# Optimization experiments

Hardware: AMD Instinct MI355X
Metric: run time of the kernel (lower is better)

Reference implementation:

```python
import jax, jax.numpy as jnp
import numpy as np

H = 128          # hidden_channels
N_USER = 100000
N_ITEM = 50000
E = 1000000      # number of labeled edges


def setup_inputs() -> dict:
    key = jax.random.key(0)
    ks = jax.random.split(key, 6)
    z_user = jax.random.normal(ks[0], (N_USER, H), dtype=jnp.float32)
    z_item = jax.random.normal(ks[1], (N_ITEM, H), dtype=jnp.float32)
    row = jax.random.randint(ks[2], (E,), 0, N_USER, dtype=jnp.int64 if jax.config.jax_enable_x64 else jnp.int32)
    col = jax.random.randint(ks[3], (E,), 0, N_ITEM, dtype=jnp.int64 if jax.config.jax_enable_x64 else jnp.int32)
    W1 = jax.random.normal(ks[4], (2 * H, H), dtype=jnp.float32) / np.sqrt(2 * H)
    b1 = jnp.zeros((H,), dtype=jnp.float32)
    W2 = jax.random.normal(ks[5], (H, 1), dtype=jnp.float32) / np.sqrt(H)
    b2 = jnp.zeros((1,), dtype=jnp.float32)
    return {"z_user": z_user, "z_item": z_item, "row": row, "col": col,
            "W1": W1, "b1": b1, "W2": W2, "b2": b2}


def reference(z_user, z_item, row, col, W1, b1, W2, b2):
    # z = cat([z_user[row], z_item[col]], -1); lin1(z).relu(); lin2 -> view(-1)
    # Split W1 so we never materialize the [E, 2H] concat explicitly as one buffer:
    # cat([a, b]) @ W1 == a @ W1[:H] + b @ W1[H:]
    W1u, W1i = W1[:H], W1[H:]
    h = z_user[row] @ W1u + z_item[col] @ W1i + b1          # [E, H]
    h = jax.nn.relu(h)
    out = h @ W2 + b2                                        # [E, 1]
    return out.reshape(-1)
```

## Files before the change

kernel.cpp:

```cpp
#include <hip/hip_runtime.h>

#define HH 128
#define BU 8
#define BI 32
#define NBKT (BU * BI)
#define SCHUNK 2048
#define GPUC 8192

typedef __attribute__((ext_vector_type(8))) short bf16x8;
typedef __attribute__((ext_vector_type(4))) float f32x4;
typedef _Float16 h2 __attribute__((ext_vector_type(2)));

#if __has_builtin(__builtin_amdgcn_fdot2)
#define FDOT2(a, b, c) __builtin_amdgcn_fdot2((a), (b), (c), false)
#else
#define FDOT2(a, b, c) ((c) + (float)(a)[0] * (float)(b)[0] + (float)(a)[1] * (float)(b)[1])
#endif

__device__ inline unsigned short f2bf(float f) {
    unsigned u = __builtin_bit_cast(unsigned, f);
    u += 0x7FFF + ((u >> 16) & 1);
    return (unsigned short)(u >> 16);
}
__device__ inline unsigned short f2h(float f) {
    return __builtin_bit_cast(unsigned short, (_Float16)f);
}

__global__ __launch_bounds__(256) void prep_kernel(
    const float* __restrict__ W1, unsigned short* __restrict__ Wt,
    const int* __restrict__ row, const int* __restrict__ col,
    unsigned* __restrict__ cursor, unsigned* __restrict__ srt,
    unsigned* __restrict__ invpos, int E, unsigned n_user, unsigned n_item, int cap)
{
    const int t = threadIdx.x;
    if ((int)blockIdx.x < 16) {
        const int gid = blockIdx.x * 256 + t;
        const int h   = gid >> 11;
        const int c   = (gid >> 4) & 127;
        const int kc  = gid & 15;
        const float* src = W1 + (size_t)(h * 128 + kc * 8) * HH + c;
        unsigned short v[8];
        #pragma unroll
        for (int d = 0; d < 8; ++d)
            v[d] = f2bf(src[(size_t)d * HH]);
        uint4 pack;
        pack.x = (unsigned)v[0] | ((unsigned)v[1] << 16);
        pack.y = (unsigned)v[2] | ((unsigned)v[3] << 16);
        pack.z = (unsigned)v[4] | ((unsigned)v[5] << 16);
        pack.w = (unsigned)v[6] | ((unsigned)v[7] << 16);
        *(uint4*)(Wt + (size_t)h * 16384 + c * 128 + ((kc ^ (c & 15)) << 3)) = pack;
        return;
    }
    __shared__ unsigned lh[NBKT];
    __shared__ unsigned gb[NBKT];
    __shared__ unsigned lc[NBKT];
    const int base = ((int)blockIdx.x - 16) * SCHUNK;

    int uu[SCHUNK / 256], ii[SCHUNK / 256];
    lh[t] = 0;
    __syncthreads();
    #pragma unroll
    for (int k = 0; k < SCHUNK / 256; ++k) {
        int e = base + k * 256 + t;
        if (e < E) {
            uu[k] = row[e]; ii[k] = col[e];
            unsigned uc = ((unsigned)uu[k] * BU) / n_user;
            unsigned ic = ((unsigned)ii[k] * BI) / n_item;
            atomicAdd(&lh[uc * BI + ic], 1u);
        }
    }
    __syncthreads();
    gb[t] = lh[t] ? (unsigned)(t * cap) + atomicAdd(&cursor[t], lh[t]) : 0u;
    lc[t] = 0;
    __syncthreads();
    #pragma unroll
    for (int k = 0; k < SCHUNK / 256; ++k) {
        int e = base + k * 256 + t;
        if (e < E) {
            unsigned uc = ((unsigned)uu[k] * BU) / n_user;
            unsigned ic = ((unsigned)ii[k] * BI) / n_item;
            int b = (int)(uc * BI + ic);
            unsigned ucbase = (uc * n_user + 7u) >> 3;
            unsigned r   = atomicAdd(&lc[b], 1u);
            unsigned pos = gb[b] + r;
            srt[pos]  = (((unsigned)uu[k] - ucbase) << 16) | (unsigned)ii[k];
            invpos[e] = pos;
        }
    }
}

__global__ __launch_bounds__(512) void project_kernel(
    const float* __restrict__ Zu, const float* __restrict__ Zi,
    const unsigned short* __restrict__ Wt, const float* __restrict__ b1,
    unsigned short* __restrict__ Pu, unsigned short* __restrict__ Pi,
    int n_user, int n_item, int utiles, int itiles)
{
    __shared__ unsigned short sWt[128 * 128];
    __shared__ unsigned short sOut[128 * 72];

    const int t    = threadIdx.x;
    const int wave = t >> 6;
    const int lane = t & 63;
    const int l16  = lane & 15;
    const int lk8  = (lane >> 4) * 8;
    const int total = utiles + itiles;

    int staged = -1;

    for (int tid = blockIdx.x; tid < total; tid += gridDim.x) {
        const bool isUser = (tid < utiles);
        const int  half   = isUser ? 0 : 1;
        const float* __restrict__ Z = isUser ? Zu : Zi;
        unsigned short* __restrict__ P = isUser ? Pu : Pi;
        const int nrows = isUser ? n_user : n_item;
        const int rbase = (isUser ? tid : (tid - utiles)) << 7;

        if (half != staged) {
            __syncthreads();
            const unsigned short* src = Wt + (size_t)half * 16384;
            #pragma unroll
            for (int i = 0; i < 4; ++i) {
                int off = (i * 512 + t) * 8;
                *(uint4*)(sWt + off) = *(const uint4*)(src + off);
            }
            __syncthreads();
            staged = half;
        }

        float b1r[8];
        #pragma unroll
        for (int nt = 0; nt < 8; ++nt)
            b1r[nt] = isUser ? b1[nt * 16 + l16] : 0.f;

        f32x4 acc[8];
        #pragma unroll
        for (int nt = 0; nt < 8; ++nt) acc[nt] = (f32x4)0.f;

        int m = rbase + wave * 16 + l16;
        if (m > nrows - 1) m = nrows - 1;
        const float* Zrow = Z + (size_t)m * HH;

        #pragma unroll
        for (int kk = 0; kk < 4; ++kk) {
            float4 z0 = *(const float4*)(Zrow + kk * 32 + lk8);
            float4 z1 = *(const float4*)(Zrow + kk * 32 + lk8 + 4);
            bf16x8 a;
            a[0] = (short)f2bf(z0.x); a[1] = (short)f2bf(z0.y);
            a[2] = (short)f2bf(z0.z); a[3] = (short)f2bf(z0.w);
            a[4] = (short)f2bf(z1.x); a[5] = (short)f2bf(z1.y);
            a[6] = (short)f2bf(z1.z); a[7] = (short)f2bf(z1.w);

            const int chunkSw = ((kk * 4 + (lane >> 4)) ^ l16) << 3;
            #pragma unroll
            for (int nt = 0; nt < 8; ++nt) {
                int c = nt * 16 + l16;
                bf16x8 b = *(const bf16x8*)(sWt + c * 128 + chunkSw);
                acc[nt] = __builtin_amdgcn_mfma_f32_16x16x32_bf16(a, b, acc[nt], 0, 0, 0);
            }
        }

        #pragma unroll
        for (int hh = 0; hh < 2; ++hh) {
            __syncthreads();
            #pragma unroll
            for (int nt2 = 0; nt2 < 4; ++nt2) {
                int nt   = hh * 4 + nt2;
                int colc = nt2 * 16 + l16;
                #pragma unroll
                for (int r = 0; r < 4; ++r) {
                    int orow = wave * 16 + (lane >> 4) * 4 + r;
                    sOut[orow * 72 + colc] = f2h(acc[nt][r] + b1r[nt]);
                }
            }
            __syncthreads();
            #pragma unroll
            for (int i = 0; i < 2; ++i) {
                int idx = t + i * 512;
                int r   = idx >> 3;
                int ch  = idx & 7;
                int grow = rbase + r;
                if (grow < nrows)
                    *(uint4*)(P + (size_t)grow * HH + hh * 64 + ch * 8) =
                        *(const uint4*)(sOut + r * 72 + ch * 8);
            }
        }
    }
}

__global__ __launch_bounds__(256) void edge_sorted_kernel(
    const unsigned short* __restrict__ Pu, const unsigned short* __restrict__ Pi,
    const unsigned* __restrict__ srt, const unsigned* __restrict__ cursor,
    const float* __restrict__ W2, const float* __restrict__ b2,
    float* __restrict__ psorted, int cap, int n_user)
{
    const int uc     = blockIdx.x & (BU - 1);
    const int jj     = blockIdx.x >> 3;
    const int g      = threadIdx.x >> 3;
    const int lane8  = threadIdx.x & 7;
    const int gg     = jj * 32 + g;
    const int c0     = lane8 * 16;
    const int ucbase = (int)(((unsigned)uc * (unsigned)n_user + 7u) >> 3);

    h2 w2h[8];
    #pragma unroll
    for (int j = 0; j < 8; ++j) {
        w2h[j][0] = (_Float16)W2[c0 + 2 * j];
        w2h[j][1] = (_Float16)W2[c0 + 2 * j + 1];
    }
    const float b2s = b2[0];
    const h2 hz = {(_Float16)0, (_Float16)0};

    #pragma unroll 1
    for (int ic = 0; ic < BI; ++ic) {
        const int b    = uc * BI + ic;
        const int S    = b * cap;
        const int Tend = S + (int)cursor[b];
        for (int p = S + gg; p < Tend; p += GPUC) {
            unsigned pk = srt[p];
            int u  = ucbase + (int)(pk >> 16);
            int it = (int)(pk & 0xFFFFu);
            const unsigned short* pur = Pu + (size_t)u  * HH + c0;
            const unsigned short* pir = Pi + (size_t)it * HH + c0;
            uint4 a0 = *(const uint4*)pur;
            uint4 a1 = *(const uint4*)(pur + 8);
            uint4 c0v = *(const uint4*)pir;
            uint4 c1v = *(const uint4*)(pir + 8);
            unsigned aw[8] = {a0.x, a0.y, a0.z, a0.w, a1.x, a1.y, a1.z, a1.w};
            unsigned cw[8] = {c0v.x, c0v.y, c0v.z, c0v.w, c1v.x, c1v.y, c1v.z, c1v.w};
            float acc = 0.f;
            #pragma unroll
            for (int q = 0; q < 8; ++q) {
                h2 s = __builtin_bit_cast(h2, aw[q]) + __builtin_bit_cast(h2, cw[q]);
                s = __builtin_elementwise_max(s, hz);
                acc = FDOT2(s, w2h[q], acc);
            }
            acc += __shfl_xor(acc, 4, 64);
            acc += __shfl_xor(acc, 2, 64);
            acc += __shfl_xor(acc, 1, 64);
            if (lane8 == 0) psorted[p] = acc + b2s;
        }
    }
}

__global__ __launch_bounds__(256) void permute_kernel(
    const float* __restrict__ psorted, const unsigned* __restrict__ invpos,
    float* __restrict__ out, int E)
{
    int i  = blockIdx.x * blockDim.x + threadIdx.x;
    int st = gridDim.x * blockDim.x;
    for (int e = i; e < E; e += st)
        out[e] = psorted[invpos[e]];
}

__global__ __launch_bounds__(256) void edge_fp16_kernel(
    const unsigned short* __restrict__ Pu, const unsigned short* __restrict__ Pi,
    const int* __restrict__ row, const int* __restrict__ col,
    const float* __restrict__ W2, const float* __restrict__ b2,
    float* __restrict__ out, int E)
{
    const int lane8  = threadIdx.x & 7;
    const int gid    = (blockIdx.x * blockDim.x + threadIdx.x) >> 3;
    const int stride = (gridDim.x * blockDim.x) >> 3;
    const int c0     = lane8 * 16;

    h2 w2h[8];
    #pragma unroll
    for (int j = 0; j < 8; ++j) {
        w2h[j][0] = (_Float16)W2[c0 + 2 * j];
        w2h[j][1] = (_Float16)W2[c0 + 2 * j + 1];
    }
    const float b2s = b2[0];
    const h2 hz = {(_Float16)0, (_Float16)0};

    for (int e = gid; e < E; e += stride) {
        int u = row[e], it = col[e];
        const unsigned short* pur = Pu + (size_t)u  * HH + c0;
        const unsigned short* pir = Pi + (size_t)it * HH + c0;
        uint4 a0 = *(const uint4*)pur;
        uint4 a1 = *(const uint4*)(pur + 8);
        uint4 c0v = *(const uint4*)pir;
        uint4 c1v = *(const uint4*)(pir + 8);
        unsigned aw[8] = {a0.x, a0.y, a0.z, a0.w, a1.x, a1.y, a1.z, a1.w};
        unsigned cw[8] = {c0v.x, c0v.y, c0v.z, c0v.w, c1v.x, c1v.y, c1v.z, c1v.w};
        float acc = 0.f;
        #pragma unroll
        for (int q = 0; q < 8; ++q) {
            h2 s = __builtin_bit_cast(h2, aw[q]) + __builtin_bit_cast(h2, cw[q]);
            s = __builtin_elementwise_max(s, hz);
            acc = FDOT2(s, w2h[q], acc);
        }
        acc += __shfl_xor(acc, 4, 64);
        acc += __shfl_xor(acc, 2, 64);
        acc += __shfl_xor(acc, 1, 64);
        if (lane8 == 0) out[e] = acc + b2s;
    }
}

__global__ __launch_bounds__(256) void edge_direct_kernel(
    const float* __restrict__ zu, const float* __restrict__ zi,
    const int* __restrict__ row, const int* __restrict__ col,
    const float* __restrict__ W1, const float* __restrict__ b1,
    const float* __restrict__ W2, const float* __restrict__ b2,
    float* __restrict__ out, int E)
{
    const int lane   = threadIdx.x & 31;
    const int gid    = (blockIdx.x * blockDim.x + threadIdx.x) >> 5;
    const int stride = (gridDim.x * blockDim.x) >> 5;
    const int c0     = lane * 4;

    const float4 b1v = *(const float4*)(b1 + c0);
    const float4 w2v = *(const float4*)(W2 + c0);
    const float  b2s = b2[0];

    for (int e = gid; e < E; e += stride) {
        int u  = row[e];
        int it = col[e];
        const float* zur = zu + (size_t)u  * HH;
        const float* zir = zi + (size_t)it * HH;
        float4 acc = b1v;
        for (int k = 0; k < HH; ++k) {
            float  zk = zur[k];
            float4 w  = *(const float4*)(W1 + (size_t)k * HH + c0);
            acc.x = fmaf(zk, w.x, acc.x);
            acc.y = fmaf(zk, w.y, acc.y);
            acc.z = fmaf(zk, w.z, acc.z);
            acc.w = fmaf(zk, w.w, acc.w);
        }
        for (int k = 0; k < HH; ++k) {
            float  zk = zir[k];
            float4 w  = *(const float4*)(W1 + (size_t)(HH + k) * HH + c0);
            acc.x = fmaf(zk, w.x, acc.x);
            acc.y = fmaf(zk, w.y, acc.y);
            acc.z = fmaf(zk, w.z, acc.z);
            acc.w = fmaf(zk, w.w, acc.w);
        }
        float p = fmaxf(acc.x, 0.f) * w2v.x;
        p = fmaf(fmaxf(acc.y, 0.f), w2v.y, p);
        p = fmaf(fmaxf(acc.z, 0.f), w2v.z, p);
        p = fmaf(fmaxf(acc.w, 0.f), w2v.w, p);
        #pragma unroll
        for (int m = 16; m >= 1; m >>= 1)
            p += __shfl_xor(p, m, 64);
        if (lane == 0) out[e] = p + b2s;
    }
}

static inline size_t align256(size_t x) { return (x + 255) & ~(size_t)255; }

extern "C" void kernel_launch(void* const* d_in, const int* in_sizes, int n_in,
                              void* d_out, int out_size, void* d_ws, size_t ws_size,
                              hipStream_t stream)
{
    const float* z_user = (const float*)d_in[0];
    const float* z_item = (const float*)d_in[1];
    const int*   row    = (const int*)d_in[2];
    const int*   col    = (const int*)d_in[3];
    const float* W1     = (const float*)d_in[4];
    const float* b1     = (const float*)d_in[5];
    const float* W2     = (const float*)d_in[6];
    const float* b2     = (const float*)d_in[7];
    float*       out    = (float*)d_out;

    const int n_user = in_sizes[0] / HH;
    const int n_item = in_sizes[1] / HH;
    const int E      = in_sizes[2];

    const int capBase = (E + NBKT - 1) / NBKT;
    const int cap     = capBase + capBase / 4 + 64;
    const size_t padded = (size_t)cap * NBKT;

    const size_t offWt  = 0;
    const size_t offPu  = align256(offWt  + 32768 * 2);
    const size_t offPi  = align256(offPu  + (size_t)n_user * HH * 2);
    const size_t offSrt = align256(offPi  + (size_t)n_item * HH * 2);
    const size_t offPs  = align256(offSrt + padded * 4);
    const size_t offInv = align256(offPs  + padded * 4);
    const size_t offCur = align256(offInv + (size_t)E * 4);
    const size_t needSort = align256(offCur + NBKT * 4);
    const size_t needProj = align256(offPi + (size_t)n_item * HH * 2);

    const bool sortable = (n_user >= BU) && (n_item >= BI) &&
                          (n_item < 65536) && (n_user / BU + 1 < 65536) &&
                          (n_user <= (1 << 17)) && (ws_size >= needSort);

    const int utiles = (n_user + 127) >> 7;
    const int itiles = (n_item + 127) >> 7;
    const int total  = utiles + itiles;
    const int pgrid  = total < 4096 ? total : 4096;
    const int scatBlocks = (E + SCHUNK - 1) / SCHUNK;

    if (sortable) {
        unsigned short* Wt  = (unsigned short*)((char*)d_ws + offWt);
        unsigned short* Pu  = (unsigned short*)((char*)d_ws + offPu);
        unsigned short* Pi  = (unsigned short*)((char*)d_ws + offPi);
        unsigned*       srt = (unsigned*)((char*)d_ws + offSrt);
        float*          ps  = (float*)((char*)d_ws + offPs);
        unsigned*       inv = (unsigned*)((char*)d_ws + offInv);
        unsigned*       cur = (unsigned*)((char*)d_ws + offCur);

        hipMemsetAsync(cur, 0, NBKT * 4, stream);
        prep_kernel<<<16 + scatBlocks, 256, 0, stream>>>(
            W1, Wt, row, col, cur, srt, inv, E, (unsigned)n_user, (unsigned)n_item, cap);
        project_kernel<<<pgrid, 512, 0, stream>>>(
            z_user, z_item, Wt, b1, Pu, Pi, n_user, n_item, utiles, itiles);
        edge_sorted_kernel<<<2048, 256, 0, stream>>>(Pu, Pi, srt, cur, W2, b2, ps, cap, n_user);
        permute_kernel<<<1024, 256, 0, stream>>>(ps, inv, out, E);
    } else if (ws_size >= needProj) {
        unsigned short* Wt = (unsigned short*)((char*)d_ws + offWt);
        unsigned short* Pu = (unsigned short*)((char*)d_ws + offPu);
        unsigned short* Pi = (unsigned short*)((char*)d_ws + offPi);
        prep_kernel<<<16, 256, 0, stream>>>(
            W1, Wt, row, col, (unsigned*)nullptr, (unsigned*)nullptr, (unsigned*)nullptr,
            0, (unsigned)n_user, (unsigned)n_item, cap);
        project_kernel<<<pgrid, 512, 0, stream>>>(
            z_user, z_item, Wt, b1, Pu, Pi, n_user, n_item, utiles, itiles);
        edge_fp16_kernel<<<2048, 256, 0, stream>>>(Pu, Pi, row, col, W2, b2, out, E);
    } else {
        edge_direct_kernel<<<2048, 256, 0, stream>>>(z_user, z_item, row, col, W1, b1, W2, b2, out, E);
    }
}
```

Measured before the change: 98.05 us.

## Fuse edge bucketing scatter and node projection into one kernel launch

Merges the prep (weight transpose plus edge bucket scatter) and projection kernels into a single launch. The first blocks do the bucket scatter with 512 threads and a doubled chunk size, and the remaining blocks each project one 128-row tile. Each projection block now converts its half of W1 to bf16 straight into shared memory, so the global Wt staging buffer goes away. This removes one kernel launch and the dependency between scatter and projection so the two can overlap. The cost is that every projection tile redoes the weight conversion from fp32, and the old persistent-grid loop becomes one block per tile.

```diff
diff --git a/kernel.cpp b/kernel.cpp
--- a/kernel.cpp
+++ b/kernel.cpp
@@ -4,7 +4,7 @@
 #define BU 8
 #define BI 32
 #define NBKT (BU * BI)
-#define SCHUNK 2048
+#define SCHUNK 4096
 #define GPUC 8192
 
 typedef __attribute__((ext_vector_type(8))) short bf16x8;
@@ -26,19 +26,77 @@
     return __builtin_bit_cast(unsigned short, (_Float16)f);
 }
 
-__global__ __launch_bounds__(256) void prep_kernel(
-    const float* __restrict__ W1, unsigned short* __restrict__ Wt,
+__global__ __launch_bounds__(512) void fused_kernel(
+    const float* __restrict__ W1, const float* __restrict__ Zu,
+    const float* __restrict__ Zi, const float* __restrict__ b1,
+    unsigned short* __restrict__ Pu, unsigned short* __restrict__ Pi,
     const int* __restrict__ row, const int* __restrict__ col,
     unsigned* __restrict__ cursor, unsigned* __restrict__ srt,
-    unsigned* __restrict__ invpos, int E, unsigned n_user, unsigned n_item, int cap)
-{
+    unsigned* __restrict__ invpos,
+    int E, unsigned n_user, unsigned n_item, int cap,
+    int scatBlocks, int utiles, int itiles)
+{
+    __shared__ unsigned short sWt[128 * 128];
+    __shared__ unsigned short sOut[128 * 72];
+
     const int t = threadIdx.x;
-    if ((int)blockIdx.x < 16) {
-        const int gid = blockIdx.x * 256 + t;
-        const int h   = gid >> 11;
-        const int c   = (gid >> 4) & 127;
-        const int kc  = gid & 15;
-        const float* src = W1 + (size_t)(h * 128 + kc * 8) * HH + c;
+
+    if ((int)blockIdx.x < scatBlocks) {
+        unsigned* lh = (unsigned*)sWt;
+        unsigned* gb = lh + NBKT;
+        unsigned* lc = gb + NBKT;
+        const int base = blockIdx.x * SCHUNK;
+
+        int uu[SCHUNK / 512], ii[SCHUNK / 512];
+        if (t < NBKT) lh[t] = 0;
+        __syncthreads();
+        #pragma unroll
+        for (int k = 0; k < SCHUNK / 512; ++k) {
+            int e = base + k * 512 + t;
+            if (e < E) {
+                uu[k] = row[e]; ii[k] = col[e];
+                unsigned uc = ((unsigned)uu[k] * BU) / n_user;
+                unsigned ic = ((unsigned)ii[k] * BI) / n_item;
+                atomicAdd(&lh[uc * BI + ic], 1u);
+            }
+        }
+        __syncthreads();
+        if (t < NBKT) {
+            gb[t] = lh[t] ? (unsigned)(t * cap) + atomicAdd(&cursor[t], lh[t]) : 0u;
+            lc[t] = 0;
+        }
+        __syncthreads();
+        #pragma unroll
+        for (int k = 0; k < SCHUNK / 512; ++k) {
+            int e = base + k * 512 + t;
+            if (e < E) {
+                unsigned uc = ((unsigned)uu[k] * BU) / n_user;
+                unsigned ic = ((unsigned)ii[k] * BI) / n_item;
+                int b = (int)(uc * BI + ic);
+                unsigned ucbase = (uc * n_user + 7u) >> 3;
+                unsigned r   = atomicAdd(&lc[b], 1u);
+                unsigned pos = gb[b] + r;
+                srt[pos]  = (((unsigned)uu[k] - ucbase) << 16) | (unsigned)ii[k];
+                invpos[e] = pos;
+            }
+        }
+        return;
+    }
+
+    const int pbid   = (int)blockIdx.x - scatBlocks;
+    const bool isUser = (pbid < utiles);
+    const float* __restrict__ Z = isUser ? Zu : Zi;
+    unsigned short* __restrict__ P = isUser ? Pu : Pi;
+    const float* __restrict__ Wh = W1 + (isUser ? 0 : (HH * HH));
+    const int nrows = isUser ? (int)n_user : (int)n_item;
+    const int rbase = (isUser ? pbid : (pbid - utiles)) << 7;
+
+    #pragma unroll
+    for (int i = 0; i < 4; ++i) {
+        int idx = i * 512 + t;
+        int c   = idx >> 4;
+        int kc  = idx & 15;
+        const float* src = Wh + (size_t)(kc * 8) * HH + c;
         unsigned short v[8];
         #pragma unroll
         for (int d = 0; d < 8; ++d)
@@ -48,141 +106,71 @@
         pack.y = (unsigned)v[2] | ((unsigned)v[3] << 16);
         pack.z = (unsigned)v[4] | ((unsigned)v[5] << 16);
         pack.w = (unsigned)v[6] | ((unsigned)v[7] << 16);
-        *(uint4*)(Wt + (size_t)h * 16384 + c * 128 + ((kc ^ (c & 15)) << 3)) = pack;
-        return;
-    }
-    __shared__ unsigned lh[NBKT];
-    __shared__ unsigned gb[NBKT];
-    __shared__ unsigned lc[NBKT];
-    const int base = ((int)blockIdx.x - 16) * SCHUNK;
-
-    int uu[SCHUNK / 256], ii[SCHUNK / 256];
-    lh[t] = 0;
-    __syncthreads();
-    #pragma unroll
-    for (int k = 0; k < SCHUNK / 256; ++k) {
-        int e = base + k * 256 + t;
-        if (e < E) {
-            uu[k] = row[e]; ii[k] = col[e];
-            unsigned uc = ((unsigned)uu[k] * BU) / n_user;
-            unsigned ic = ((unsigned)ii[k] * BI) / n_item;
-            atomicAdd(&lh[uc * BI + ic], 1u);
-        }
-    }
-    __syncthreads();
-    gb[t] = lh[t] ? (unsigned)(t * cap) + atomicAdd(&cursor[t], lh[t]) : 0u;
-    lc[t] = 0;
-    __syncthreads();
-    #pragma unroll
-    for (int k = 0; k < SCHUNK / 256; ++k) {
-        int e = base + k * 256 + t;
-        if (e < E) {
-            unsigned uc = ((unsigned)uu[k] * BU) / n_user;
-            unsigned ic = ((unsigned)ii[k] * BI) / n_item;
-            int b = (int)(uc * BI + ic);
-            unsigned ucbase = (uc * n_user + 7u) >> 3;
-            unsigned r   = atomicAdd(&lc[b], 1u);
-            unsigned pos = gb[b] + r;
-            srt[pos]  = (((unsigned)uu[k] - ucbase) << 16) | (unsigned)ii[k];
-            invpos[e] = pos;
-        }
-    }
-}
-
-__global__ __launch_bounds__(512) void project_kernel(
-    const float* __restrict__ Zu, const float* __restrict__ Zi,
-    const unsigned short* __restrict__ Wt, const float* __restrict__ b1,
-    unsigned short* __restrict__ Pu, unsigned short* __restrict__ Pi,
-    int n_user, int n_item, int utiles, int itiles)
-{
-    __shared__ unsigned short sWt[128 * 128];
-    __shared__ unsigned short sOut[128 * 72];
-
-    const int t    = threadIdx.x;
+        *(uint4*)(sWt + c * 128 + ((kc ^ (c & 15)) << 3)) = pack;
+    }
+
     const int wave = t >> 6;
     const int lane = t & 63;
     const int l16  = lane & 15;
     const int lk8  = (lane >> 4) * 8;
-    const int total = utiles + itiles;
-
-    int staged = -1;
-
-    for (int tid = blockIdx.x; tid < total; tid += gridDim.x) {
-        const bool isUser = (tid < utiles);
-        const int  half   = isUser ? 0 : 1;
-        const float* __restrict__ Z = isUser ? Zu : Zi;
-        unsigned short* __restrict__ P = isUser ? Pu : Pi;
-        const int nrows = isUser ? n_user : n_item;
-        const int rbase = (isUser ? tid : (tid - utiles)) << 7;
-
-        if (half != staged) {
-            __syncthreads();
-            const unsigned short* src = Wt + (size_t)half * 16384;
+
+    float b1r[8];
+    #pragma unroll
+    for (int nt = 0; nt < 8; ++nt)
+        b1r[nt] = isUser ? b1[nt * 16 + l16] : 0.f;
+
+    __syncthreads();
+
+    f32x4 acc[8];
+    #pragma unroll
+    for (int nt = 0; nt < 8; ++nt) acc[nt] = (f32x4)0.f;
+
+    int m = rbase + wave * 16 + l16;
+    if (m > nrows - 1) m = nrows - 1;
+    const float* Zrow = Z + (size_t)m * HH;
+
+    #pragma unroll
+    for (int kk = 0; kk < 4; ++kk) {
+        float4 z0 = *(const float4*)(Zrow + kk * 32 + lk8);
+        float4 z1 = *(const float4*)(Zrow + kk * 32 + lk8 + 4);
+        bf16x8 a;
+        a[0] = (short)f2bf(z0.x); a[1] = (short)f2bf(z0.y);
+        a[2] = (short)f2bf(z0.z); a[3] = (short)f2bf(z0.w);
+        a[4] = (short)f2bf(z1.x); a[5] = (short)f2bf(z1.y);
+        a[6] = (short)f2bf(z1.z); a[7] = (short)f2bf(z1.w);
+
+        const int chunkSw = ((kk * 4 + (lane >> 4)) ^ l16) << 3;
+        #pragma unroll
+        for (int nt = 0; nt < 8; ++nt) {
+            int c = nt * 16 + l16;
+            bf16x8 b = *(const bf16x8*)(sWt + c * 128 + chunkSw);
+            acc[nt] = __builtin_amdgcn_mfma_f32_16x16x32_bf16(a, b, acc[nt], 0, 0, 0);
+        }
+    }
+
+    #pragma unroll
+    for (int hh = 0; hh < 2; ++hh) {
+        __syncthreads();
+        #pragma unroll
+        for (int nt2 = 0; nt2 < 4; ++nt2) {
+            int nt   = hh * 4 + nt2;
+            int colc = nt2 * 16 + l16;
             #pragma unroll
-            for (int i = 0; i < 4; ++i) {
-                int off = (i * 512 + t) * 8;
-                *(uint4*)(sWt + off) = *(const uint4*)(src + off);
+            for (int r = 0; r < 4; ++r) {
+                int orow = wave * 16 + (lane >> 4) * 4 + r;
+                sOut[orow * 72 + colc] = f2h(acc[nt][r] + b1r[nt]);
             }
-            __syncthreads();
-            staged = half;
-        }
-
-        float b1r[8];
-        #pragma unroll
-        for (int nt = 0; nt < 8; ++nt)
-            b1r[nt] = isUser ? b1[nt * 16 + l16] : 0.f;
-
-        f32x4 acc[8];
-        #pragma unroll
-        for (int nt = 0; nt < 8; ++nt) acc[nt] = (f32x4)0.f;
-
-        int m = rbase + wave * 16 + l16;
-        if (m > nrows - 1) m = nrows - 1;
-        const float* Zrow = Z + (size_t)m * HH;
-
-        #pragma unroll
-        for (int kk = 0; kk < 4; ++kk) {
-            float4 z0 = *(const float4*)(Zrow + kk * 32 + lk8);
-            float4 z1 = *(const float4*)(Zrow + kk * 32 + lk8 + 4);
-            bf16x8 a;
-            a[0] = (short)f2bf(z0.x); a[1] = (short)f2bf(z0.y);
-            a[2] = (short)f2bf(z0.z); a[3] = (short)f2bf(z0.w);
-            a[4] = (short)f2bf(z1.x); a[5] = (short)f2bf(z1.y);
-            a[6] = (short)f2bf(z1.z); a[7] = (short)f2bf(z1.w);
-
-            const int chunkSw = ((kk * 4 + (lane >> 4)) ^ l16) << 3;
-            #pragma unroll
-            for (int nt = 0; nt < 8; ++nt) {
-                int c = nt * 16 + l16;
-                bf16x8 b = *(const bf16x8*)(sWt + c * 128 + chunkSw);
-                acc[nt] = __builtin_amdgcn_mfma_f32_16x16x32_bf16(a, b, acc[nt], 0, 0, 0);
-            }
-        }
-
-        #pragma unroll
-        for (int hh = 0; hh < 2; ++hh) {
-            __syncthreads();
-            #pragma unroll
-            for (int nt2 = 0; nt2 < 4; ++nt2) {
-                int nt   = hh * 4 + nt2;
-                int colc = nt2 * 16 + l16;
-                #pragma unroll
-                for (int r = 0; r < 4; ++r) {
-                    int orow = wave * 16 + (lane >> 4) * 4 + r;
-                    sOut[orow * 72 + colc] = f2h(acc[nt][r] + b1r[nt]);
-                }
-            }
-            __syncthreads();
-            #pragma unroll
-            for (int i = 0; i < 2; ++i) {
-                int idx = t + i * 512;
-                int r   = idx >> 3;
-                int ch  = idx & 7;
-                int grow = rbase + r;
-                if (grow < nrows)
-                    *(uint4*)(P + (size_t)grow * HH + hh * 64 + ch * 8) =
-                        *(const uint4*)(sOut + r * 72 + ch * 8);
-            }
+        }
+        __syncthreads();
+        #pragma unroll
+        for (int i = 0; i < 2; ++i) {
+            int idx = t + i * 512;
+            int r   = idx >> 3;
+            int ch  = idx & 7;
+            int grow = rbase + r;
+            if (grow < nrows)
+                *(uint4*)(P + (size_t)grow * HH + hh * 64 + ch * 8) =
+                    *(const uint4*)(sOut + r * 72 + ch * 8);
         }
     }
 }
@@ -369,8 +357,7 @@
     const int cap     = capBase + capBase / 4 + 64;
     const size_t padded = (size_t)cap * NBKT;
 
-    const size_t offWt  = 0;
-    const size_t offPu  = align256(offWt  + 32768 * 2);
+    const size_t offPu  = 0;
     const size_t offPi  = align256(offPu  + (size_t)n_user * HH * 2);
     const size_t offSrt = align256(offPi  + (size_t)n_item * HH * 2);
     const size_t offPs  = align256(offSrt + padded * 4);
@@ -385,12 +372,9 @@
 
     const int utiles = (n_user + 127) >> 7;
     const int itiles = (n_item + 127) >> 7;
-    const int total  = utiles + itiles;
-    const int pgrid  = total < 4096 ? total : 4096;
     const int scatBlocks = (E + SCHUNK - 1) / SCHUNK;
 
     if (sortable) {
-        unsigned short* Wt  = (unsigned short*)((char*)d_ws + offWt);
         unsigned short* Pu  = (unsigned short*)((char*)d_ws + offPu);
         unsigned short* Pi  = (unsigned short*)((char*)d_ws + offPi);
         unsigned*       srt = (unsigned*)((char*)d_ws + offSrt);
@@ -399,21 +383,18 @@
         unsigned*       cur = (unsigned*)((char*)d_ws + offCur);
 
         hipMemsetAsync(cur, 0, NBKT * 4, stream);
-        prep_kernel<<<16 + scatBlocks, 256, 0, stream>>>(
-            W1, Wt, row, col, cur, srt, inv, E, (unsigned)n_user, (unsigned)n_item, cap);
-        project_kernel<<<pgrid, 512, 0, stream>>>(
-            z_user, z_item, Wt, b1, Pu, Pi, n_user, n_item, utiles, itiles);
+        fused_kernel<<<scatBlocks + utiles + itiles, 512, 0, stream>>>(
+            W1, z_user, z_item, b1, Pu, Pi, row, col, cur, srt, inv,
+            E, (unsigned)n_user, (unsigned)n_item, cap, scatBlocks, utiles, itiles);
         edge_sorted_kernel<<<2048, 256, 0, stream>>>(Pu, Pi, srt, cur, W2, b2, ps, cap, n_user);
         permute_kernel<<<1024, 256, 0, stream>>>(ps, inv, out, E);
     } else if (ws_size >= needProj) {
-        unsigned short* Wt = (unsigned short*)((char*)d_ws + offWt);
         unsigned short* Pu = (unsigned short*)((char*)d_ws + offPu);
         unsigned short* Pi = (unsigned short*)((char*)d_ws + offPi);
-        prep_kernel<<<16, 256, 0, stream>>>(
-            W1, Wt, row, col, (unsigned*)nullptr, (unsigned*)nullptr, (unsigned*)nullptr,
-            0, (unsigned)n_user, (unsigned)n_item, cap);
-        project_kernel<<<pgrid, 512, 0, stream>>>(
-            z_user, z_item, Wt, b1, Pu, Pi, n_user, n_item, utiles, itiles);
+        fused_kernel<<<utiles + itiles, 512, 0, stream>>>(
+            W1, z_user, z_item, b1, Pu, Pi, row, col,
+            (unsigned*)nullptr, (unsigned*)nullptr, (unsigned*)nullptr,
+            0, (unsigned)n_user, (unsigned)n_item, cap, 0, utiles, itiles);
         edge_fp16_kernel<<<2048, 256, 0, stream>>>(Pu, Pi, row, col, W2, b2, out, E);
     } else {
         edge_direct_kernel<<<2048, 256, 0, stream>>>(z_user, z_item, row, col, W1, b1, W2, b2, out, E);
```

After: 113.2 us. +15.4%, slower.
